# Kernel tuning notes

Hardware: AMD Instinct MI355X
Metric: run time of the kernel (lower is better)

The kernel has to match this reference:

```python
import jax, jax.numpy as jnp
import numpy as np

RADIUS = 9.0
GROUPS = 4
BLK = 64  # row block for streaming the N x N pairwise convolution


def leaky(x):
    return jnp.where(x >= 0, x, 0.2 * x)


def group_norm(x, gamma, beta, eps=1e-5):
    # x: (N, C); matches torch.nn.GroupNorm(GROUPS, C) applied to (1, C, N)
    N, C = x.shape
    xg = x.T.reshape(GROUPS, (C // GROUPS) * N)
    m = xg.mean(axis=1, keepdims=True)
    v = ((xg - m) ** 2).mean(axis=1, keepdims=True)
    xg = (xg - m) / jnp.sqrt(v + eps)
    return xg.reshape(C, N).T * gamma + beta


def tangent_vectors(n):
    # Duff et al. orthonormal tangent basis; n: (N,3) unit normals -> (N,2,3)
    x, y, z = n[:, 0], n[:, 1], n[:, 2]
    s = jnp.where(z >= 0, 1.0, -1.0)
    a = -1.0 / (s + z)
    b = x * y * a
    uv = jnp.stack([1 + s * x * x * a, s * b, -s * x, b, s + y * y * a, -y], axis=-1)
    return uv.reshape(-1, 2, 3)


def load_mesh(xyz, normals, weights):
    # Build oriented local frames nuv (N,3,3) as in dMaSIFConv_seg.load_mesh
    p = xyz / RADIUS
    uv = tangent_vectors(normals)                  # (N,2,3)
    diff = p[None, :, :] - p[:, None, :]           # (N,N,3): x_j - x_i
    d2 = jnp.sum(diff * diff, axis=-1)             # (N,N)
    cos = normals @ normals.T                      # (N,N)
    window = jnp.exp(-d2 * (2.0 - cos) ** 2)       # pseudo-geodesic Gaussian
    X = jnp.einsum('ikd,ijd->ijk', uv, diff)       # (N,N,2) tangent coords
    ov = jnp.einsum('ij,j,ijk->ik', window, weights[:, 0], X) + 1e-5  # (N,2)
    nrm = jnp.maximum(jnp.linalg.norm(ov, axis=-1, keepdims=True), 1e-12)
    ov = ov / nrm                                  # F.normalize
    ex, ey = ov[:, :1], ov[:, 1:]
    u, v = uv[:, 0, :], uv[:, 1, :]
    return jnp.stack([normals, ex * u + ey * v, -ey * u + ex * v], axis=1)


def dmasif_conv(points, nuv, feats,
                ni_w1, ni_b1, ni_w2, ni_b2, gn_in_g, gn_in_b,
                cv_a1, cv_b1, cv_a2, cv_b2,
                no_w1, no_b1, no_w2, no_b2, gn_out_g, gn_out_b):
    N = points.shape[0]
    H = ni_w1.shape[0]
    O = no_w1.shape[0]
    # net_in + GroupNorm
    h = leaky(feats @ ni_w1.T + ni_b1)
    h = leaky(h @ ni_w2.T + ni_b2)
    h = group_norm(h, gn_in_g, gn_in_b)            # (N,H)
    p = points / (np.sqrt(2.0) * RADIUS)
    n = jax.lax.stop_gradient(nuv[:, 0, :])        # normals detached in window

    p_blk = p.reshape(-1, BLK, 3)
    n_blk = n.reshape(-1, BLK, 3)
    nuv_blk = nuv.reshape(-1, BLK, 3, 3)

    @jax.checkpoint
    def step(carry, blk):
        pi, ni, nuvi = blk                                  # (B,3),(B,3),(B,3,3)
        diff = p[None, :, :] - pi[:, None, :]               # (B,N,3)
        d2 = jnp.sum(diff * diff, axis=-1)                  # (B,N)
        window = jnp.exp(-d2 * (2.0 - ni @ n.T) ** 2)       # (B,N)
        X = jnp.einsum('bkd,bnd->bnk', nuvi, diff)          # (B,N,3) local coords
        g = jax.nn.relu(jnp.einsum('bnk,ck->bnc', X, cv_a1) + cv_b1)  # (B,N,8)
        M = jax.nn.relu(jnp.einsum('bnc,fc->bnf', g, cv_a2) + cv_b2)  # (B,N,H*O)
        M = M.reshape(BLK, N, O, H)
        out = jnp.einsum('bn,bnoh,nh->bo', window, M, h)    # (B,O)
        return carry, out

    _, outs = jax.lax.scan(step, None, (p_blk, n_blk, nuv_blk))
    y = outs.reshape(N, O)
    y = leaky(y @ no_w1.T + no_b1)
    y = leaky(y @ no_w2.T + no_b2)
    return group_norm(y, gn_out_g, gn_out_b)


def setup_inputs() -> dict:
    key = jax.random.key(0)
    ks = jax.random.split(key, 32)
    N, I, U, H, O, C = 4096, 16, 16, 16, 16, 8
    nrm = jax.random.normal(ks[1], (N, 3), dtype=jnp.float32)
    nrm = nrm / jnp.linalg.norm(nrm, axis=-1, keepdims=True)
    w = lambda k, sh: 0.1 * jax.random.normal(k, sh, dtype=jnp.float32)
    return {
        'surface_xyz': 10.0 * jax.random.normal(ks[0], (N, 3), dtype=jnp.float32),
        'surface_normals': nrm,
        'features': jax.random.normal(ks[2], (N, I), dtype=jnp.float32),
        'os_w1': w(ks[3], (U, I)), 'os_b1': w(ks[4], (U,)),
        'os_w2': w(ks[5], (1, U)), 'os_b2': w(ks[6], (1,)),
        'ni_w1': w(ks[7], (H, I)), 'ni_b1': w(ks[8], (H,)),
        'ni_w2': w(ks[9], (H, H)), 'ni_b2': w(ks[10], (H,)),
        'gn_in_g': jnp.ones((H,), jnp.float32), 'gn_in_b': jnp.zeros((H,), jnp.float32),
        'cv_a1': w(ks[11], (C, 3)), 'cv_b1': w(ks[12], (C,)),
        'cv_a2': w(ks[13], (H * O, C)), 'cv_b2': w(ks[14], (H * O,)),
        'no_w1': w(ks[15], (O, H)), 'no_b1': w(ks[16], (O,)),
        'no_w2': w(ks[17], (O, O)), 'no_b2': w(ks[18], (O,)),
        'gn_out_g': jnp.ones((O,), jnp.float32), 'gn_out_b': jnp.zeros((O,), jnp.float32),
        'll_w1': w(ks[19], (O, O)), 'll_b1': w(ks[20], (O,)),
        'll_w2': w(ks[21], (O, O)), 'll_b2': w(ks[22], (O,)),
        'lt_w': w(ks[23], (O, I)), 'lt_b': w(ks[24], (O,)),
    }


def reference(surface_xyz, surface_normals, features,
              os_w1, os_b1, os_w2, os_b2,
              ni_w1, ni_b1, ni_w2, ni_b2, gn_in_g, gn_in_b,
              cv_a1, cv_b1, cv_a2, cv_b2,
              no_w1, no_b1, no_w2, no_b2, gn_out_g, gn_out_b,
              ll_w1, ll_b1, ll_w2, ll_b2, lt_w, lt_b):
    # orientation scores: Linear -> LeakyReLU(0.2) -> Linear
    scores = leaky(features @ os_w1.T + os_b1) @ os_w2.T + os_b2  # (N,1)
    nuv = load_mesh(surface_xyz, surface_normals, scores)
    # dMaSIFConv_seg forward, n_layers = 1
    x_i = dmasif_conv(surface_xyz, nuv, features,
                      ni_w1, ni_b1, ni_w2, ni_b2, gn_in_g, gn_in_b,
                      cv_a1, cv_b1, cv_a2, cv_b2,
                      no_w1, no_b1, no_w2, no_b2, gn_out_g, gn_out_b)
    x_i = jax.nn.relu(x_i @ ll_w1.T + ll_b1) @ ll_w2.T + ll_b2  # linear_layers[0]
    x = features @ lt_w.T + lt_b                                 # linear_transform[0]
    return x + x_i
```

## Files before the change

kernel.cpp:

```cpp
#include <hip/hip_runtime.h>

#define NP 4096
#define NJC 32
#define JCH (NP / NJC)
#define HR  12

typedef const float* fp;

using half4  = __attribute__((ext_vector_type(4))) __fp16;
using fp16x2 = __attribute__((ext_vector_type(2))) __fp16;
using f32x4  = __attribute__((ext_vector_type(4))) float;

__device__ __forceinline__ float lk(float x) { return x >= 0.f ? x : 0.2f * x; }

__device__ __forceinline__ unsigned int pkrtz(float a, float b) {
    fp16x2 h = __builtin_amdgcn_cvt_pkrtz(a, b);
    unsigned int u; __builtin_memcpy(&u, &h, 4); return u;
}
__device__ __forceinline__ fp16x2 u2h(unsigned int u) {
    fp16x2 h; __builtin_memcpy(&h, &u, 4); return h;
}
__device__ __forceinline__ fp16x2 pkmax0(fp16x2 a, fp16x2 z) {
    fp16x2 d;
    asm("v_pk_max_f16 %0, %1, %2" : "=v"(d) : "v"(a), "v"(z));
    return d;
}

#define OFF_ACC   0
#define OFF_OV    16
#define OFF_CONV  (16 + 2*NP)
#define ZERO_FLTS (16 + 2*NP + 16*NP)
#define OFF_SC    ZERO_FLTS
#define OFF_UV    (OFF_SC  + NP)
#define OFF_P9    (OFF_UV  + 6*NP)
#define OFF_NRM   (OFF_P9  + 3*NP)
#define OFF_HPRE  (OFF_NRM + 3*NP)
#define OFF_HNRM  (OFF_HPRE+ 16*NP)
#define OFF_NUV   (OFF_HNRM+ 16*NP)
#define OFF_Y2    (OFF_NUV + 9*NP)
#define WS_FLTS   (OFF_Y2  + 16*NP)

__global__ __launch_bounds__(256) void k_prep(
    fp xyz, fp nrm, fp feats,
    fp osw1, fp osb1, fp osw2, fp osb2,
    fp niw1, fp nib1, fp niw2, fp nib2,
    float* __restrict__ ws)
{
    const int i = blockIdx.x * 256 + threadIdx.x;

    float f[16];
#pragma unroll
    for (int c = 0; c < 16; c++) f[c] = feats[i * 16 + c];

    float sc = osb2[0];
#pragma unroll
    for (int u = 0; u < 16; u++) {
        float a = osb1[u];
#pragma unroll
        for (int c = 0; c < 16; c++) a += osw1[u * 16 + c] * f[c];
        sc += osw2[u] * lk(a);
    }
    ws[OFF_SC + i] = sc;

    float h1[16];
#pragma unroll
    for (int u = 0; u < 16; u++) {
        float a = nib1[u];
#pragma unroll
        for (int c = 0; c < 16; c++) a += niw1[u * 16 + c] * f[c];
        h1[u] = lk(a);
    }
    float h2[16];
#pragma unroll
    for (int u = 0; u < 16; u++) {
        float a = nib2[u];
#pragma unroll
        for (int c = 0; c < 16; c++) a += niw2[u * 16 + c] * h1[c];
        h2[u] = lk(a);
        ws[OFF_HPRE + i * 16 + u] = h2[u];
    }

#pragma unroll
    for (int g = 0; g < 4; g++) {
        float s = 0.f, ss = 0.f;
#pragma unroll
        for (int k = 0; k < 4; k++) { float v = h2[g * 4 + k]; s += v; ss += v * v; }
#pragma unroll
        for (int off = 32; off > 0; off >>= 1) {
            s  += __shfl_down(s,  off);
            ss += __shfl_down(ss, off);
        }
        if ((threadIdx.x & 63) == 0) {
            atomicAdd(&ws[OFF_ACC + g],     s);
            atomicAdd(&ws[OFF_ACC + 4 + g], ss);
        }
    }

    float nx = nrm[i * 3], ny = nrm[i * 3 + 1], nz = nrm[i * 3 + 2];
    float s  = (nz >= 0.f) ? 1.f : -1.f;
    float a  = -1.f / (s + nz);
    float b  = nx * ny * a;
    float ux = 1.f + s * nx * nx * a, uy = s * b,            uz = -s * nx;
    float vx = b,                     vy = s + ny * ny * a,  vz = -ny;
    ws[OFF_UV + i * 6 + 0] = ux; ws[OFF_UV + i * 6 + 1] = uy; ws[OFF_UV + i * 6 + 2] = uz;
    ws[OFF_UV + i * 6 + 3] = vx; ws[OFF_UV + i * 6 + 4] = vy; ws[OFF_UV + i * 6 + 5] = vz;
    const float IR = 1.f / 9.f;
    ws[OFF_P9 + i * 3 + 0] = xyz[i * 3 + 0] * IR;
    ws[OFF_P9 + i * 3 + 1] = xyz[i * 3 + 1] * IR;
    ws[OFF_P9 + i * 3 + 2] = xyz[i * 3 + 2] * IR;
    ws[OFF_NRM + i * 3 + 0] = nx;
    ws[OFF_NRM + i * 3 + 1] = ny;
    ws[OFF_NRM + i * 3 + 2] = nz;
}

__global__ __launch_bounds__(256) void k_mesh(float* __restrict__ ws)
{
    __shared__ float sp[3][512];
    __shared__ float sn[3][512];
    __shared__ float ssc[512];
    __shared__ float red[256][2];

    const int tid = threadIdx.x;
    const int ib = blockIdx.x >> 3, jc = blockIdx.x & 7;
    const int il = tid & 63, sub = tid >> 6;
    const int i = ib * 64 + il;
    const int j0 = jc * 512;

    for (int t = tid; t < 512; t += 256) {
        int j = j0 + t;
        sp[0][t] = ws[OFF_P9 + j * 3];     sp[1][t] = ws[OFF_P9 + j * 3 + 1];  sp[2][t] = ws[OFF_P9 + j * 3 + 2];
        sn[0][t] = ws[OFF_NRM + j * 3];    sn[1][t] = ws[OFF_NRM + j * 3 + 1]; sn[2][t] = ws[OFF_NRM + j * 3 + 2];
        ssc[t]   = ws[OFF_SC + j];
    }
    __syncthreads();

    const float pix = ws[OFF_P9 + i * 3], piy = ws[OFF_P9 + i * 3 + 1], piz = ws[OFF_P9 + i * 3 + 2];
    const float nix = ws[OFF_NRM + i * 3], niy = ws[OFF_NRM + i * 3 + 1], niz = ws[OFF_NRM + i * 3 + 2];
    const float ux = ws[OFF_UV + i * 6],     uy = ws[OFF_UV + i * 6 + 1], uz = ws[OFF_UV + i * 6 + 2];
    const float vx = ws[OFF_UV + i * 6 + 3], vy = ws[OFF_UV + i * 6 + 4], vz = ws[OFF_UV + i * 6 + 5];

    float ov0 = 0.f, ov1 = 0.f;
#pragma unroll 4
    for (int t = 0; t < 128; t++) {
        int j = sub * 128 + t;
        float dx = sp[0][j] - pix, dy = sp[1][j] - piy, dz = sp[2][j] - piz;
        float d2 = dx * dx + dy * dy + dz * dz;
        float cs = nix * sn[0][j] + niy * sn[1][j] + niz * sn[2][j];
        float tt = 2.f - cs;
        float w  = __expf(-d2 * tt * tt) * ssc[j];
        ov0 += w * (ux * dx + uy * dy + uz * dz);
        ov1 += w * (vx * dx + vy * dy + vz * dz);
    }
    red[tid][0] = ov0; red[tid][1] = ov1;
    __syncthreads();
    if (sub == 0) {
        float a = ov0 + red[64 + il][0] + red[128 + il][0] + red[192 + il][0];
        float b = ov1 + red[64 + il][1] + red[128 + il][1] + red[192 + il][1];
        atomicAdd(&ws[OFF_OV + i * 2],     a);
        atomicAdd(&ws[OFF_OV + i * 2 + 1], b);
    }
}

__global__ __launch_bounds__(256) void k_fin(float* __restrict__ ws, fp gng, fp gnb)
{
    const int i = blockIdx.x * 256 + threadIdx.x;

    float o0 = ws[OFF_OV + i * 2]     + 1e-5f;
    float o1 = ws[OFF_OV + i * 2 + 1] + 1e-5f;
    float nr = fmaxf(sqrtf(o0 * o0 + o1 * o1), 1e-12f);
    float ex = o0 / nr, ey = o1 / nr;

    const float ux = ws[OFF_UV + i * 6],     uy = ws[OFF_UV + i * 6 + 1], uz = ws[OFF_UV + i * 6 + 2];
    const float vx = ws[OFF_UV + i * 6 + 3], vy = ws[OFF_UV + i * 6 + 4], vz = ws[OFF_UV + i * 6 + 5];
    const float nx = ws[OFF_NRM + i * 3], ny = ws[OFF_NRM + i * 3 + 1], nz = ws[OFF_NRM + i * 3 + 2];

    ws[OFF_NUV + i * 9 + 0] = nx;
    ws[OFF_NUV + i * 9 + 1] = ny;
    ws[OFF_NUV + i * 9 + 2] = nz;
    ws[OFF_NUV + i * 9 + 3] =  ex * ux + ey * vx;
    ws[OFF_NUV + i * 9 + 4] =  ex * uy + ey * vy;
    ws[OFF_NUV + i * 9 + 5] =  ex * uz + ey * vz;
    ws[OFF_NUV + i * 9 + 6] = -ey * ux + ex * vx;
    ws[OFF_NUV + i * 9 + 7] = -ey * uy + ex * vy;
    ws[OFF_NUV + i * 9 + 8] = -ey * uz + ex * vz;

    const float invM = 1.f / (4.f * NP);
#pragma unroll
    for (int c = 0; c < 16; c++) {
        int g = c >> 2;
        float m   = ws[OFF_ACC + g] * invM;
        float var = ws[OFF_ACC + 4 + g] * invM - m * m;
        float inv = rsqrtf(var + 1e-5f);
        ws[OFF_HNRM + i * 16 + c] =
            (ws[OFF_HPRE + i * 16 + c] - m) * inv * gng[c] + gnb[c];
    }
}

__global__ __launch_bounds__(256, 4) void k_conv(
    const float* __restrict__ ws,
    const float* __restrict__ cva1, const float* __restrict__ cvb1,
    const float* __restrict__ A2,   const float* __restrict__ B2,
    float* __restrict__ conv)
{
    __shared__ float4 sP[JCH];
    __shared__ float4 sN[JCH];
    __shared__ __align__(16) unsigned int sH2[JCH * HR];

    const int tid  = threadIdx.x;
    const int ib   = blockIdx.x >> 5;
    const int jc   = blockIdx.x & 31;
    const int j0   = jc * JCH;
    const int lane = tid & 63;
    const int wv   = tid >> 6;
    const int o    = lane & 15;
    const int quad = lane >> 4;
    const float IVS2 = 0.70710678118654752f;

    if (tid < JCH) {
        const int t = tid;
        const int j = j0 + t;
        sP[t] = make_float4(ws[OFF_P9 + j * 3] * IVS2,
                            ws[OFF_P9 + j * 3 + 1] * IVS2,
                            ws[OFF_P9 + j * 3 + 2] * IVS2, 0.f);
        sN[t] = make_float4(ws[OFF_NRM + j * 3],
                            ws[OFF_NRM + j * 3 + 1],
                            ws[OFF_NRM + j * 3 + 2], 0.f);
        const float4* hs = (const float4*)(ws + OFF_HNRM + j * 16);
        float4 h0 = hs[0], h1 = hs[1], h2 = hs[2], h3 = hs[3];
        uint4 w0, w1;
        w0.x = pkrtz(h0.x, h0.y); w0.y = pkrtz(h0.z, h0.w);
        w0.z = pkrtz(h1.x, h1.y); w0.w = pkrtz(h1.z, h1.w);
        w1.x = pkrtz(h2.x, h2.y); w1.y = pkrtz(h2.z, h2.w);
        w1.z = pkrtz(h3.x, h3.y); w1.w = pkrtz(h3.z, h3.w);
        *(uint4*)(sH2 + t * HR)     = w0;
        *(uint4*)(sH2 + t * HR + 4) = w1;
    }

    half4 Bf[16];
#pragma unroll
    for (int t = 0; t < 16; t++) {
        half4 v = {(__fp16)0.f, (__fp16)0.f, (__fp16)0.f, (__fp16)0.f};
        const float* row = A2 + (o * 16 + t) * 8;
        if (quad == 0) {
#pragma unroll
            for (int c = 0; c < 4; c++) v[c] = (__fp16)row[c];
        } else if (quad == 1) {
#pragma unroll
            for (int c = 0; c < 4; c++) v[c] = (__fp16)row[4 + c];
        } else if (quad == 2) {
            v[0] = (__fp16)B2[o * 16 + t];
        }
        Bf[t] = v;
    }

    float a1[24], b1c[8];
#pragma unroll
    for (int k = 0; k < 24; k++) a1[k] = cva1[k];
#pragma unroll
    for (int k = 0; k < 8; k++)  b1c[k] = cvb1[k];

    __syncthreads();

    const f32x4 zc = {0.f, 0.f, 0.f, 0.f};
    const fp16x2 h2z = {(__fp16)0.f, (__fp16)0.f};
    const int o4 = o << 2;

#pragma unroll 1
    for (int ii = 0; ii < 16; ii++) {
        const int i = ib * 64 + wv * 16 + ii;
        const float pix = ws[OFF_P9 + i * 3 + 0] * IVS2;
        const float piy = ws[OFF_P9 + i * 3 + 1] * IVS2;
        const float piz = ws[OFF_P9 + i * 3 + 2] * IVS2;
        float r[9];
#pragma unroll
        for (int k = 0; k < 9; k++) r[k] = ws[OFF_NUV + i * 9 + k];

        float accO = 0.f;

#pragma unroll 1
        for (int jg = 0; jg < JCH / 64; jg++) {
            const int jl = jg * 64 + lane;
            const float4 pj = sP[jl];
            const float4 nj = sN[jl];
            const float dx = pj.x - pix, dy = pj.y - piy, dz = pj.z - piz;
            const float d2 = dx * dx + dy * dy + dz * dz;
            const float cs = r[0] * nj.x + r[1] * nj.y + r[2] * nj.z;
            const float tt = 2.f - cs;
            const float wwin = __expf(-d2 * tt * tt);
            const float X0 = r[0] * dx + r[1] * dy + r[2] * dz;
            const float X1 = r[3] * dx + r[4] * dy + r[5] * dz;
            const float X2 = r[6] * dx + r[7] * dy + r[8] * dz;
            float g[8];
#pragma unroll
            for (int c = 0; c < 8; c++)
                g[c] = fmaxf(a1[c * 3] * X0 + a1[c * 3 + 1] * X1 +
                             a1[c * 3 + 2] * X2 + b1c[c], 0.f);
            const int wg0 = (int)pkrtz(wwin * g[0], wwin * g[1]);
            const int wg1 = (int)pkrtz(wwin * g[2], wwin * g[3]);
            const int wg2 = (int)pkrtz(wwin * g[4], wwin * g[5]);
            const int wg3 = (int)pkrtz(wwin * g[6], wwin * g[7]);
            const int whp = (int)pkrtz(wwin, 0.f);

#pragma unroll 1
            for (int tau = 0; tau < 4; tau++) {
                const int srcb = tau * 64 + o4;
                const unsigned u0 = (unsigned)__builtin_amdgcn_ds_bpermute(srcb, wg0);
                const unsigned u1 = (unsigned)__builtin_amdgcn_ds_bpermute(srcb, wg1);
                const unsigned u2 = (unsigned)__builtin_amdgcn_ds_bpermute(srcb, wg2);
                const unsigned u3 = (unsigned)__builtin_amdgcn_ds_bpermute(srcb, wg3);
                const unsigned uw = (unsigned)__builtin_amdgcn_ds_bpermute(srcb, whp);
                uint2 av;
                av.x = (quad == 0) ? u0 : (quad == 1) ? u2 : (quad == 2) ? uw : 0u;
                av.y = (quad == 0) ? u1 : (quad == 1) ? u3 : 0u;
                half4 Af; __builtin_memcpy(&Af, &av, 8);

#pragma unroll
                for (int hq = 0; hq < 2; hq++) {
                    fp16x2 P[16];
#pragma unroll
                    for (int q2 = 0; q2 < 4; q2++) {
                        const int q = hq * 4 + q2;
                        f32x4 C0 = __builtin_amdgcn_mfma_f32_16x16x16f16(Af, Bf[2 * q],     zc, 0, 0, 0);
                        f32x4 C1 = __builtin_amdgcn_mfma_f32_16x16x16f16(Af, Bf[2 * q + 1], zc, 0, 0, 0);
#pragma unroll
                        for (int r2 = 0; r2 < 4; r2++) {
                            fp16x2 pp = __builtin_amdgcn_cvt_pkrtz(C0[r2], C1[r2]);
                            P[r2 * 4 + q2] = pkmax0(pp, h2z);
                        }
                    }
#pragma unroll
                    for (int r2 = 0; r2 < 4; r2++) {
                        const unsigned int* hr =
                            sH2 + (jg * 64 + tau * 16 + quad * 4 + r2) * HR + hq * 4;
                        const uint4 ha = *(const uint4*)hr;
                        accO = __builtin_amdgcn_fdot2(P[r2 * 4 + 0], u2h(ha.x), accO, false);
                        accO = __builtin_amdgcn_fdot2(P[r2 * 4 + 1], u2h(ha.y), accO, false);
                        accO = __builtin_amdgcn_fdot2(P[r2 * 4 + 2], u2h(ha.z), accO, false);
                        accO = __builtin_amdgcn_fdot2(P[r2 * 4 + 3], u2h(ha.w), accO, false);
                    }
                }
            }
        }

        accO += __shfl_xor(accO, 16, 64);
        accO += __shfl_xor(accO, 32, 64);
        if (lane < 16) atomicAdd(&conv[i * 16 + o], accO);
    }
}

__global__ __launch_bounds__(256) void k_post1(
    float* __restrict__ ws, fp now1, fp nob1, fp now2, fp nob2)
{
    const int i = blockIdx.x * 256 + threadIdx.x;
    float cv[16];
#pragma unroll
    for (int o = 0; o < 16; o++) cv[o] = ws[OFF_CONV + i * 16 + o];

    float y1[16];
#pragma unroll
    for (int u = 0; u < 16; u++) {
        float a = nob1[u];
#pragma unroll
        for (int k = 0; k < 16; k++) a += now1[u * 16 + k] * cv[k];
        y1[u] = lk(a);
    }
    float y2[16];
#pragma unroll
    for (int u = 0; u < 16; u++) {
        float a = nob2[u];
#pragma unroll
        for (int k = 0; k < 16; k++) a += now2[u * 16 + k] * y1[k];
        y2[u] = lk(a);
        ws[OFF_Y2 + i * 16 + u] = y2[u];
    }
#pragma unroll
    for (int g = 0; g < 4; g++) {
        float s = 0.f, ss = 0.f;
#pragma unroll
        for (int k = 0; k < 4; k++) { float v = y2[g * 4 + k]; s += v; ss += v * v; }
#pragma unroll
        for (int off = 32; off > 0; off >>= 1) {
            s  += __shfl_down(s,  off);
            ss += __shfl_down(ss, off);
        }
        if ((threadIdx.x & 63) == 0) {
            atomicAdd(&ws[OFF_ACC + 8 + g],  s);
            atomicAdd(&ws[OFF_ACC + 12 + g], ss);
        }
    }
}

__global__ __launch_bounds__(256) void k_post2(
    const float* __restrict__ ws, fp feats, fp gg, fp gb,
    fp llw1, fp llb1, fp llw2, fp llb2, fp ltw, fp ltb,
    float* __restrict__ out)
{
    const int i = blockIdx.x * 256 + threadIdx.x;
    const float invM = 1.f / (4.f * NP);

    float z[16];
#pragma unroll
    for (int c = 0; c < 16; c++) {
        int g = c >> 2;
        float m   = ws[OFF_ACC + 8 + g] * invM;
        float var = ws[OFF_ACC + 12 + g] * invM - m * m;
        float inv = rsqrtf(var + 1e-5f);
        z[c] = (ws[OFF_Y2 + i * 16 + c] - m) * inv * gg[c] + gb[c];
    }
    float r1[16];
#pragma unroll
    for (int o = 0; o < 16; o++) {
        float a = llb1[o];
#pragma unroll
        for (int k = 0; k < 16; k++) a += llw1[o * 16 + k] * z[k];
        r1[o] = fmaxf(a, 0.f);
    }
    float f[16];
#pragma unroll
    for (int c = 0; c < 16; c++) f[c] = feats[i * 16 + c];
#pragma unroll
    for (int o = 0; o < 16; o++) {
        float a = llb2[o];
#pragma unroll
        for (int k = 0; k < 16; k++) a += llw2[o * 16 + k] * r1[k];
        float x = ltb[o];
#pragma unroll
        for (int k = 0; k < 16; k++) x += ltw[o * 16 + k] * f[k];
        out[i * 16 + o] = x + a;
    }
}

extern "C" void kernel_launch(void* const* d_in, const int* in_sizes, int n_in,
                              void* d_out, int out_size, void* d_ws, size_t ws_size,
                              hipStream_t stream)
{
    fp xyz  = (fp)d_in[0];
    fp nrm  = (fp)d_in[1];
    fp fts  = (fp)d_in[2];
    fp osw1 = (fp)d_in[3],  osb1 = (fp)d_in[4],  osw2 = (fp)d_in[5],  osb2 = (fp)d_in[6];
    fp niw1 = (fp)d_in[7],  nib1 = (fp)d_in[8],  niw2 = (fp)d_in[9],  nib2 = (fp)d_in[10];
    fp gng  = (fp)d_in[11], gnb  = (fp)d_in[12];
    fp cva1 = (fp)d_in[13], cvb1 = (fp)d_in[14], cva2 = (fp)d_in[15], cvb2 = (fp)d_in[16];
    fp now1 = (fp)d_in[17], nob1 = (fp)d_in[18], now2 = (fp)d_in[19], nob2 = (fp)d_in[20];
    fp gog  = (fp)d_in[21], gob  = (fp)d_in[22];
    fp llw1 = (fp)d_in[23], llb1 = (fp)d_in[24], llw2 = (fp)d_in[25], llb2 = (fp)d_in[26];
    fp ltw  = (fp)d_in[27], ltb  = (fp)d_in[28];

    float* ws = (float*)d_ws;

    (void)hipMemsetAsync(d_ws, 0, (size_t)ZERO_FLTS * sizeof(float), stream);
    k_prep<<<NP / 256, 256, 0, stream>>>(xyz, nrm, fts,
                                         osw1, osb1, osw2, osb2,
                                         niw1, nib1, niw2, nib2, ws);
    k_mesh<<<512, 256, 0, stream>>>(ws);
    k_fin<<<NP / 256, 256, 0, stream>>>(ws, gng, gnb);
    k_conv<<<64 * NJC, 256, 0, stream>>>(ws, cva1, cvb1, cva2, cvb2, ws + OFF_CONV);
    k_post1<<<NP / 256, 256, 0, stream>>>(ws, now1, nob1, now2, nob2);
    k_post2<<<NP / 256, 256, 0, stream>>>(ws, fts, gog, gob,
                                          llw1, llb1, llw2, llb2, ltw, ltb,
                                          (float*)d_out);
}
```

Measured before the change: 473.6 us.

## Stage MFMA A-operand through LDS and split fdot2 accumulators

Instead of five ds_bpermute ops per tau plus selects to build the MFMA A fragment, each lane writes its packed weighted-gate values into a per-wave LDS buffer once per j-group, and lanes read their A fragment with one 8-byte LDS load per tau. The single serial fdot2 accumulator is split into four independent chains to shorten the dependency latency. The extra LDS buffer raises shared memory use, so launch bounds drop from 4 to 3 blocks per SIMD, which may reduce occupancy.

New measurement: 479.5 us. About the same (+1.2%).

```diff
diff --git a/kernel.cpp b/kernel.cpp
--- a/kernel.cpp
+++ b/kernel.cpp
@@ -4,6 +4,7 @@
 #define NJC 32
 #define JCH (NP / NJC)
 #define HR  12
+#define WGS 12
 
 typedef const float* fp;
 
@@ -196,7 +197,7 @@
     }
 }
 
-__global__ __launch_bounds__(256, 4) void k_conv(
+__global__ __launch_bounds__(256, 3) void k_conv(
     const float* __restrict__ ws,
     const float* __restrict__ cva1, const float* __restrict__ cvb1,
     const float* __restrict__ A2,   const float* __restrict__ B2,
@@ -205,6 +206,7 @@
     __shared__ float4 sP[JCH];
     __shared__ float4 sN[JCH];
     __shared__ __align__(16) unsigned int sH2[JCH * HR];
+    __shared__ __align__(16) unsigned int sWG[4 * 64 * WGS];
 
     const int tid  = threadIdx.x;
     const int ib   = blockIdx.x >> 5;
@@ -263,7 +265,8 @@
 
     const f32x4 zc = {0.f, 0.f, 0.f, 0.f};
     const fp16x2 h2z = {(__fp16)0.f, (__fp16)0.f};
-    const int o4 = o << 2;
+    unsigned int* wb = sWG + wv * (64 * WGS) + lane * WGS;
+    const unsigned int* rbase = sWG + wv * (64 * WGS) + (quad << 1);
 
 #pragma unroll 1
     for (int ii = 0; ii < 16; ii++) {
@@ -275,7 +278,7 @@
 #pragma unroll
         for (int k = 0; k < 9; k++) r[k] = ws[OFF_NUV + i * 9 + k];
 
-        float accO = 0.f;
+        float acc0 = 0.f, acc1 = 0.f, acc2 = 0.f, acc3 = 0.f;
 
 #pragma unroll 1
         for (int jg = 0; jg < JCH / 64; jg++) {
@@ -295,23 +298,17 @@
             for (int c = 0; c < 8; c++)
                 g[c] = fmaxf(a1[c * 3] * X0 + a1[c * 3 + 1] * X1 +
                              a1[c * 3 + 2] * X2 + b1c[c], 0.f);
-            const int wg0 = (int)pkrtz(wwin * g[0], wwin * g[1]);
-            const int wg1 = (int)pkrtz(wwin * g[2], wwin * g[3]);
-            const int wg2 = (int)pkrtz(wwin * g[4], wwin * g[5]);
-            const int wg3 = (int)pkrtz(wwin * g[6], wwin * g[7]);
-            const int whp = (int)pkrtz(wwin, 0.f);
+            uint4 wgv;
+            wgv.x = pkrtz(wwin * g[0], wwin * g[1]);
+            wgv.y = pkrtz(wwin * g[2], wwin * g[3]);
+            wgv.z = pkrtz(wwin * g[4], wwin * g[5]);
+            wgv.w = pkrtz(wwin * g[6], wwin * g[7]);
+            *(uint4*)wb       = wgv;
+            *(uint4*)(wb + 4) = make_uint4(pkrtz(wwin, 0.f), 0u, 0u, 0u);
 
 #pragma unroll 1
             for (int tau = 0; tau < 4; tau++) {
-                const int srcb = tau * 64 + o4;
-                const unsigned u0 = (unsigned)__builtin_amdgcn_ds_bpermute(srcb, wg0);
-                const unsigned u1 = (unsigned)__builtin_amdgcn_ds_bpermute(srcb, wg1);
-                const unsigned u2 = (unsigned)__builtin_amdgcn_ds_bpermute(srcb, wg2);
-                const unsigned u3 = (unsigned)__builtin_amdgcn_ds_bpermute(srcb, wg3);
-                const unsigned uw = (unsigned)__builtin_amdgcn_ds_bpermute(srcb, whp);
-                uint2 av;
-                av.x = (quad == 0) ? u0 : (quad == 1) ? u2 : (quad == 2) ? uw : 0u;
-                av.y = (quad == 0) ? u1 : (quad == 1) ? u3 : 0u;
+                const uint2 av = *(const uint2*)(rbase + (tau * 16 + o) * WGS);
                 half4 Af; __builtin_memcpy(&Af, &av, 8);
 
 #pragma unroll
@@ -328,20 +325,37 @@
                             P[r2 * 4 + q2] = pkmax0(pp, h2z);
                         }
                     }
-#pragma unroll
-                    for (int r2 = 0; r2 < 4; r2++) {
-                        const unsigned int* hr =
-                            sH2 + (jg * 64 + tau * 16 + quad * 4 + r2) * HR + hq * 4;
-                        const uint4 ha = *(const uint4*)hr;
-                        accO = __builtin_amdgcn_fdot2(P[r2 * 4 + 0], u2h(ha.x), accO, false);
-                        accO = __builtin_amdgcn_fdot2(P[r2 * 4 + 1], u2h(ha.y), accO, false);
-                        accO = __builtin_amdgcn_fdot2(P[r2 * 4 + 2], u2h(ha.z), accO, false);
-                        accO = __builtin_amdgcn_fdot2(P[r2 * 4 + 3], u2h(ha.w), accO, false);
+                    {
+                        const unsigned int* h0p = sH2 + (jg * 64 + tau * 16 + quad * 4 + 0) * HR + hq * 4;
+                        const unsigned int* h1p = h0p + HR;
+                        const unsigned int* h2p = h1p + HR;
+                        const unsigned int* h3p = h2p + HR;
+                        const uint4 ha0 = *(const uint4*)h0p;
+                        const uint4 ha1 = *(const uint4*)h1p;
+                        const uint4 ha2 = *(const uint4*)h2p;
+                        const uint4 ha3 = *(const uint4*)h3p;
+                        acc0 = __builtin_amdgcn_fdot2(P[0],  u2h(ha0.x), acc0, false);
+                        acc0 = __builtin_amdgcn_fdot2(P[1],  u2h(ha0.y), acc0, false);
+                        acc0 = __builtin_amdgcn_fdot2(P[2],  u2h(ha0.z), acc0, false);
+                        acc0 = __builtin_amdgcn_fdot2(P[3],  u2h(ha0.w), acc0, false);
+                        acc1 = __builtin_amdgcn_fdot2(P[4],  u2h(ha1.x), acc1, false);
+                        acc1 = __builtin_amdgcn_fdot2(P[5],  u2h(ha1.y), acc1, false);
+                        acc1 = __builtin_amdgcn_fdot2(P[6],  u2h(ha1.z), acc1, false);
+                        acc1 = __builtin_amdgcn_fdot2(P[7],  u2h(ha1.w), acc1, false);
+                        acc2 = __builtin_amdgcn_fdot2(P[8],  u2h(ha2.x), acc2, false);
+                        acc2 = __builtin_amdgcn_fdot2(P[9],  u2h(ha2.y), acc2, false);
+                        acc2 = __builtin_amdgcn_fdot2(P[10], u2h(ha2.z), acc2, false);
+                        acc2 = __builtin_amdgcn_fdot2(P[11], u2h(ha2.w), acc2, false);
+                        acc3 = __builtin_amdgcn_fdot2(P[12], u2h(ha3.x), acc3, false);
+                        acc3 = __builtin_amdgcn_fdot2(P[13], u2h(ha3.y), acc3, false);
+                        acc3 = __builtin_amdgcn_fdot2(P[14], u2h(ha3.z), acc3, false);
+                        acc3 = __builtin_amdgcn_fdot2(P[15], u2h(ha3.w), acc3, false);
                     }
                 }
             }
         }
 
+        float accO = (acc0 + acc1) + (acc2 + acc3);
         accO += __shfl_xor(accO, 16, 64);
         accO += __shfl_xor(accO, 32, 64);
         if (lane < 16) atomicAdd(&conv[i * 16 + o], accO);
```
